# Kernel tuning notes

Hardware: AMD Instinct MI355X
Metric: run time of the kernel (lower is better)

Reference implementation:

```python
import jax, jax.numpy as jnp
import numpy as np

EPS = 1e-06

def elu_feature_map(x):
    # elu(x) + 1, matching torch.nn.functional.elu default alpha=1
    return jax.nn.elu(x) + 1.0

def setup_inputs() -> dict:
    key = jax.random.key(0)
    k1, k2, k3 = jax.random.split(key, 3)
    n, L, h, e = 4, 8192, 8, 64
    queries = jax.random.normal(k1, (n, L, h, e), dtype=jnp.float32)
    keys = jax.random.normal(k2, (n, L, h, e), dtype=jnp.float32)
    values = jax.random.normal(k3, (n, L, h, e), dtype=jnp.float32)
    return {"queries": queries, "keys": keys, "values": values}

def reference(queries, keys, values):
    n, l, h, e = queries.shape
    softmax_temp = e ** (-0.25)
    q = elu_feature_map(queries * softmax_temp)   # [n, l, h, e]
    k = elu_feature_map(keys * softmax_temp)      # [n, s, h, e]
    # kv: sum over sequence of outer products k (x) v -> [n, h, d_v, e]
    kv = jnp.einsum('nshd,nshm->nhmd', k, values)
    # normalizer z = 1 / (q . sum_s k)
    z = 1.0 / (jnp.einsum('nlhd,nhd->nlh', q, k.sum(axis=1)) + EPS)
    v = jnp.einsum('nlhd,nhmd,nlh->nlhm', q, kv, z)
    return v
```

## Files before the change

kernel.cpp:

```cpp
#include <hip/hip_runtime.h>

#define N_      4
#define L_      8192
#define H_      8
#define E_      64
#define NH_     (N_ * H_)
#define STRIDE_ (H_ * E_)
#define SPLIT_  32
#define RPB_    (L_ / SPLIT_)
#define CHR_    64
#define NCHK_   (RPB_ / CHR_)

typedef short bf16x8 __attribute__((ext_vector_type(8)));
typedef float f32x16 __attribute__((ext_vector_type(16)));

__device__ __forceinline__ float featmap(float x) {
    float xs = x * 0.35355339059327373f;
    return xs > 0.0f ? xs + 1.0f : __expf(xs);
}
__device__ __forceinline__ unsigned short f2bf(float f) {
    union { float f; unsigned u; } c{f};
    unsigned r = c.u + 0x7FFFu + ((c.u >> 16) & 1u);
    return (unsigned short)(r >> 16);
}
__device__ __forceinline__ unsigned cvt_pk_bf16(float lo, float hi) {
    unsigned r;
    asm("v_cvt_pk_bf16_f32 %0, %1, %2" : "=v"(r) : "v"(lo), "v"(hi));
    return r;
}
__device__ __forceinline__ int swz_slot(int d, int sp4) {
    return (sp4 ^ (d & 7) ^ ((d >> 2) & 7)) & 7;
}

__global__ __launch_bounds__(256) void la_kv(
    const float* __restrict__ keys, const float* __restrict__ values,
    float* __restrict__ pkv, float* __restrict__ pks)
{
    const int blk = blockIdx.x;
    const int nh = blk / SPLIT_, chunk = blk % SPLIT_;
    const int n = nh / H_, h = nh % H_;
    const int t = threadIdx.x, l = t & 63;
    const int w = t >> 6, wd = w >> 1, wm = w & 1;
    const int lm = l & 31, lh = l >> 5;
    const int pr = t >> 3, c = t & 7;

    __shared__ unsigned Kb[2][CHR_][32];
    __shared__ unsigned Vb[2][CHR_][32];

    f32x16 acc = {0,0,0,0,0,0,0,0,0,0,0,0,0,0,0,0};
    float ksp[8] = {0.f,0.f,0.f,0.f,0.f,0.f,0.f,0.f};

    const size_t base = (size_t)n * (L_ * H_ * E_) + (size_t)h * E_;
    const size_t rbase = base + (size_t)(chunk * RPB_ + 2 * pr) * STRIDE_ + 4 * c;

    float4 kr0 = *(const float4*)(keys + rbase);
    float4 kr1 = *(const float4*)(keys + rbase + 32);
    float4 kr2 = *(const float4*)(keys + rbase + STRIDE_);
    float4 kr3 = *(const float4*)(keys + rbase + STRIDE_ + 32);
    float4 vr0 = *(const float4*)(values + rbase);
    float4 vr1 = *(const float4*)(values + rbase + 32);
    float4 vr2 = *(const float4*)(values + rbase + STRIDE_);
    float4 vr3 = *(const float4*)(values + rbase + STRIDE_ + 32);

    #pragma unroll
    for (int ch = 0; ch < NCHK_; ++ch) {
        const int buf = ch & 1;
        float a0[4] = {kr0.x, kr0.y, kr0.z, kr0.w};
        float a1[4] = {kr1.x, kr1.y, kr1.z, kr1.w};
        float a2[4] = {kr2.x, kr2.y, kr2.z, kr2.w};
        float a3[4] = {kr3.x, kr3.y, kr3.z, kr3.w};
        float b0[4] = {vr0.x, vr0.y, vr0.z, vr0.w};
        float b1[4] = {vr1.x, vr1.y, vr1.z, vr1.w};
        float b2[4] = {vr2.x, vr2.y, vr2.z, vr2.w};
        float b3[4] = {vr3.x, vr3.y, vr3.z, vr3.w};

        #pragma unroll
        for (int i = 0; i < 4; ++i) {
            const float f0 = featmap(a0[i]), f1 = featmap(a1[i]);
            const float f2 = featmap(a2[i]), f3 = featmap(a3[i]);
            ksp[i]     += f0 + f2;
            ksp[4 + i] += f1 + f3;
            const int dl = 4 * c + i, dh = 32 + 4 * c + i;
            const int wl = swz_slot(dl, pr >> 2) * 4 + (pr & 3);
            const int wh = swz_slot(dh, pr >> 2) * 4 + (pr & 3);
            Kb[buf][dl][wl] = cvt_pk_bf16(f0, f2);
            Kb[buf][dh][wh] = cvt_pk_bf16(f1, f3);
            Vb[buf][dl][wl] = cvt_pk_bf16(b0[i], b2[i]);
            Vb[buf][dh][wh] = cvt_pk_bf16(b1[i], b3[i]);
        }

        __syncthreads();

        if (ch + 1 < NCHK_) {
            const size_t nb = rbase + (size_t)(ch + 1) * CHR_ * STRIDE_;
            kr0 = *(const float4*)(keys + nb);
            kr1 = *(const float4*)(keys + nb + 32);
            kr2 = *(const float4*)(keys + nb + STRIDE_);
            kr3 = *(const float4*)(keys + nb + STRIDE_ + 32);
            vr0 = *(const float4*)(values + nb);
            vr1 = *(const float4*)(values + nb + 32);
            vr2 = *(const float4*)(values + nb + STRIDE_);
            vr3 = *(const float4*)(values + nb + STRIDE_ + 32);
        }

        const int rk = 32 * wd + lm, rv = 32 * wm + lm;
        #pragma unroll
        for (int m = 0; m < 4; ++m) {
            const int sa = ((2 * m + lh) ^ (lm & 7) ^ (lm >> 2)) & 7;
            bf16x8 af = *(const bf16x8*)&Kb[buf][rk][sa * 4];
            bf16x8 bv = *(const bf16x8*)&Vb[buf][rv][sa * 4];
            acc = __builtin_amdgcn_mfma_f32_32x32x16_bf16(af, bv, acc, 0, 0, 0);
        }
    }

    float* dst = pkv + (size_t)blk * (E_ * E_);
    #pragma unroll
    for (int r = 0; r < 16; ++r) {
        const int ro = (r & 3) + 8 * (r >> 2) + 4 * lh;
        dst[(32 * wd + ro) * E_ + 32 * wm + lm] = acc[r];
    }

    __syncthreads();
    float* ksb = (float*)&Kb[0][0][0];
    *(float4*)&ksb[t * 8]     = make_float4(ksp[0], ksp[1], ksp[2], ksp[3]);
    *(float4*)&ksb[t * 8 + 4] = make_float4(ksp[4], ksp[5], ksp[6], ksp[7]);
    __syncthreads();
    if (t < E_) {
        const int cc = (t & 31) >> 2, e = (t >> 5) * 4 + (t & 3);
        float s = 0.f;
        #pragma unroll
        for (int pp = 0; pp < 32; ++pp) s += ksb[(pp * 8 + cc) * 8 + e];
        pks[(size_t)blk * E_ + t] = s;
    }
}

__global__ __launch_bounds__(256) void la_reduce(
    const float* __restrict__ pkv, const float* __restrict__ pks,
    unsigned short* __restrict__ kvt, float* __restrict__ ksum)
{
    const int b = blockIdx.x, nh = b >> 4, sl = b & 15;
    const int e = sl * 256 + threadIdx.x;
    const float* src = pkv + (size_t)nh * SPLIT_ * (E_ * E_) + e;
    float s = 0.f;
    #pragma unroll
    for (int c = 0; c < SPLIT_; ++c) s += src[(size_t)c * (E_ * E_)];
    const int d = e >> 6, m = e & 63;
    kvt[(size_t)nh * (E_ * E_) + m * E_ + d] = f2bf(s);

    if (sl == 0 && threadIdx.x < E_) {
        const float* sp = pks + (size_t)nh * SPLIT_ * E_ + threadIdx.x;
        float ss = 0.f;
        #pragma unroll
        for (int c = 0; c < SPLIT_; ++c) ss += sp[c * E_];
        ksum[nh * E_ + threadIdx.x] = ss;
    }
}

__global__ __launch_bounds__(256) void la_out(
    const float* __restrict__ q, const unsigned short* __restrict__ kvt,
    const float* __restrict__ ksum, float* __restrict__ out)
{
    const int blk = blockIdx.x, nh = blk >> 5, tile = blk & 31;
    const int n = nh / H_, h = nh % H_;
    const int t = threadIdx.x, l = t & 63, w = t >> 6;
    const int lm = l & 31, lh = l >> 5;

    __shared__ float zbuf[4][32];

    const unsigned short* kb = kvt + (size_t)nh * (E_ * E_);
    const float* ks = ksum + nh * E_;

    bf16x8 bfr[4][2];
    float4 kr[4][2];
    #pragma unroll
    for (int st = 0; st < 4; ++st) {
        #pragma unroll
        for (int c = 0; c < 2; ++c)
            bfr[st][c] = *(const bf16x8*)&kb[(32 * c + lm) * E_ + st * 16 + 8 * lh];
        kr[st][0] = *(const float4*)&ks[st * 16 + 8 * lh];
        kr[st][1] = *(const float4*)&ks[st * 16 + 8 * lh + 4];
    }

    const size_t base = (size_t)n * (L_ * H_ * E_) + (size_t)h * E_;

    #pragma unroll
    for (int bnd = 0; bnd < 2; ++bnd) {
        const int l0 = tile * 256 + w * 64 + bnd * 32;
        const float* qp = q + base + (size_t)(l0 + lm) * STRIDE_ + 8 * lh;

        float4 qa[4], qb[4];
        #pragma unroll
        for (int st = 0; st < 4; ++st) {
            qa[st] = *(const float4*)(qp + st * 16);
            qb[st] = *(const float4*)(qp + st * 16 + 4);
        }

        float zd = 0.f;
        bf16x8 af[4];
        #pragma unroll
        for (int st = 0; st < 4; ++st) {
            const float f0 = featmap(qa[st].x), f1 = featmap(qa[st].y),
                        f2 = featmap(qa[st].z), f3 = featmap(qa[st].w);
            const float g0 = featmap(qb[st].x), g1 = featmap(qb[st].y),
                        g2 = featmap(qb[st].z), g3 = featmap(qb[st].w);
            zd += f0 * kr[st][0].x + f1 * kr[st][0].y + f2 * kr[st][0].z + f3 * kr[st][0].w
                + g0 * kr[st][1].x + g1 * kr[st][1].y + g2 * kr[st][1].z + g3 * kr[st][1].w;
            union { bf16x8 v; unsigned u[4]; } a;
            a.u[0] = cvt_pk_bf16(f0, f1);
            a.u[1] = cvt_pk_bf16(f2, f3);
            a.u[2] = cvt_pk_bf16(g0, g1);
            a.u[3] = cvt_pk_bf16(g2, g3);
            af[st] = a.v;
        }
        zd += __shfl_xor(zd, 32);
        const float z = 1.0f / (zd + 1e-6f);
        if (l < 32) zbuf[w][l] = z;
        __builtin_amdgcn_wave_barrier();

        f32x16 c0 = {0,0,0,0,0,0,0,0,0,0,0,0,0,0,0,0};
        f32x16 c1 = {0,0,0,0,0,0,0,0,0,0,0,0,0,0,0,0};
        #pragma unroll
        for (int st = 0; st < 4; ++st) {
            c0 = __builtin_amdgcn_mfma_f32_32x32x16_bf16(af[st], bfr[st][0], c0, 0, 0, 0);
            c1 = __builtin_amdgcn_mfma_f32_32x32x16_bf16(af[st], bfr[st][1], c1, 0, 0, 0);
        }

        float* op = out + base + (size_t)l0 * STRIDE_ + lm;
        #pragma unroll
        for (int r = 0; r < 16; ++r) {
            const int ro = (r & 3) + 8 * (r >> 2) + 4 * lh;
            const float zz = zbuf[w][ro];
            op[(size_t)ro * STRIDE_]      = c0[r] * zz;
            op[(size_t)ro * STRIDE_ + 32] = c1[r] * zz;
        }
        __builtin_amdgcn_wave_barrier();
    }
}

extern "C" void kernel_launch(void* const* d_in, const int* in_sizes, int n_in,
                              void* d_out, int out_size, void* d_ws, size_t ws_size,
                              hipStream_t stream) {
    (void)in_sizes; (void)n_in; (void)out_size; (void)ws_size;
    const float* qq = (const float*)d_in[0];
    const float* kk = (const float*)d_in[1];
    const float* vv = (const float*)d_in[2];
    float* outp = (float*)d_out;
    float* ws   = (float*)d_ws;

    float* pkv = ws;
    float* pks = ws + (size_t)NH_ * SPLIT_ * (E_ * E_);
    unsigned short* kvt = (unsigned short*)(pks + (size_t)NH_ * SPLIT_ * E_);
    float* ksm = (float*)(kvt + (size_t)NH_ * (E_ * E_));

    la_kv<<<NH_ * SPLIT_, 256, 0, stream>>>(kk, vv, pkv, pks);
    la_reduce<<<NH_ * 16, 256, 0, stream>>>(pkv, pks, kvt, ksm);
    la_out<<<NH_ * 32, 256, 0, stream>>>(qq, kvt, ksm, outp);
}
```

Baseline: 67.82 us.

## Deepen register prefetch to two chunks and halve sequence split

Keys and values are now prefetched two chunks ahead into a double-buffered register array instead of one chunk ahead, giving global loads more time to land before use. The sequence split per (n,h) is halved, so each block handles twice as many rows and fewer partial KV matrices are written and reduced. The cost is more live registers, which can lower occupancy, and fewer blocks in flight across the GPU.

```diff
diff --git a/kernel.cpp b/kernel.cpp
--- a/kernel.cpp
+++ b/kernel.cpp
@@ -6,9 +6,9 @@
 #define E_      64
 #define NH_     (N_ * H_)
 #define STRIDE_ (H_ * E_)
-#define SPLIT_  32
+#define CHR_    64
+#define SPLIT_  16
 #define RPB_    (L_ / SPLIT_)
-#define CHR_    64
 #define NCHK_   (RPB_ / CHR_)
 
 typedef short bf16x8 __attribute__((ext_vector_type(8)));
@@ -53,26 +53,33 @@
     const size_t base = (size_t)n * (L_ * H_ * E_) + (size_t)h * E_;
     const size_t rbase = base + (size_t)(chunk * RPB_ + 2 * pr) * STRIDE_ + 4 * c;
 
-    float4 kr0 = *(const float4*)(keys + rbase);
-    float4 kr1 = *(const float4*)(keys + rbase + 32);
-    float4 kr2 = *(const float4*)(keys + rbase + STRIDE_);
-    float4 kr3 = *(const float4*)(keys + rbase + STRIDE_ + 32);
-    float4 vr0 = *(const float4*)(values + rbase);
-    float4 vr1 = *(const float4*)(values + rbase + 32);
-    float4 vr2 = *(const float4*)(values + rbase + STRIDE_);
-    float4 vr3 = *(const float4*)(values + rbase + STRIDE_ + 32);
+    float4 kr[2][4], vr[2][4];
+
+#define LOADCH(CH, B) {                                                       \
+    const size_t nb = rbase + (size_t)(CH) * CHR_ * STRIDE_;                  \
+    kr[B][0] = *(const float4*)(keys + nb);                                   \
+    kr[B][1] = *(const float4*)(keys + nb + 32);                              \
+    kr[B][2] = *(const float4*)(keys + nb + STRIDE_);                         \
+    kr[B][3] = *(const float4*)(keys + nb + STRIDE_ + 32);                    \
+    vr[B][0] = *(const float4*)(values + nb);                                 \
+    vr[B][1] = *(const float4*)(values + nb + 32);                            \
+    vr[B][2] = *(const float4*)(values + nb + STRIDE_);                       \
+    vr[B][3] = *(const float4*)(values + nb + STRIDE_ + 32); }
+
+    LOADCH(0, 0);
+    LOADCH(1, 1);
 
     #pragma unroll
     for (int ch = 0; ch < NCHK_; ++ch) {
         const int buf = ch & 1;
-        float a0[4] = {kr0.x, kr0.y, kr0.z, kr0.w};
-        float a1[4] = {kr1.x, kr1.y, kr1.z, kr1.w};
-        float a2[4] = {kr2.x, kr2.y, kr2.z, kr2.w};
-        float a3[4] = {kr3.x, kr3.y, kr3.z, kr3.w};
-        float b0[4] = {vr0.x, vr0.y, vr0.z, vr0.w};
-        float b1[4] = {vr1.x, vr1.y, vr1.z, vr1.w};
-        float b2[4] = {vr2.x, vr2.y, vr2.z, vr2.w};
-        float b3[4] = {vr3.x, vr3.y, vr3.z, vr3.w};
+        float a0[4] = {kr[buf][0].x, kr[buf][0].y, kr[buf][0].z, kr[buf][0].w};
+        float a1[4] = {kr[buf][1].x, kr[buf][1].y, kr[buf][1].z, kr[buf][1].w};
+        float a2[4] = {kr[buf][2].x, kr[buf][2].y, kr[buf][2].z, kr[buf][2].w};
+        float a3[4] = {kr[buf][3].x, kr[buf][3].y, kr[buf][3].z, kr[buf][3].w};
+        float b0[4] = {vr[buf][0].x, vr[buf][0].y, vr[buf][0].z, vr[buf][0].w};
+        float b1[4] = {vr[buf][1].x, vr[buf][1].y, vr[buf][1].z, vr[buf][1].w};
+        float b2[4] = {vr[buf][2].x, vr[buf][2].y, vr[buf][2].z, vr[buf][2].w};
+        float b3[4] = {vr[buf][3].x, vr[buf][3].y, vr[buf][3].z, vr[buf][3].w};
 
         #pragma unroll
         for (int i = 0; i < 4; ++i) {
@@ -91,17 +98,7 @@
 
         __syncthreads();
 
-        if (ch + 1 < NCHK_) {
-            const size_t nb = rbase + (size_t)(ch + 1) * CHR_ * STRIDE_;
-            kr0 = *(const float4*)(keys + nb);
-            kr1 = *(const float4*)(keys + nb + 32);
-            kr2 = *(const float4*)(keys + nb + STRIDE_);
-            kr3 = *(const float4*)(keys + nb + STRIDE_ + 32);
-            vr0 = *(const float4*)(values + nb);
-            vr1 = *(const float4*)(values + nb + 32);
-            vr2 = *(const float4*)(values + nb + STRIDE_);
-            vr3 = *(const float4*)(values + nb + STRIDE_ + 32);
-        }
+        if (ch + 2 < NCHK_) LOADCH(ch + 2, buf);
 
         const int rk = 32 * wd + lm, rv = 32 * wm + lm;
         #pragma unroll
@@ -112,6 +109,7 @@
             acc = __builtin_amdgcn_mfma_f32_32x32x16_bf16(af, bv, acc, 0, 0, 0);
         }
     }
+#undef LOADCH
 
     float* dst = pkv + (size_t)blk * (E_ * E_);
     #pragma unroll
```

Result: faster. 64.02 us (-5.6%).
